# Performance work log

Hardware: AMD Instinct MI355X
Metric: run time of the kernel (lower is better)

## Reference

```python
import jax, jax.numpy as jnp
import numpy as np

HIDDEN = 64
N_NODES = 100000
N_EDGES = 1250000
EDGE_FEAT = 13


def setup_inputs() -> dict:
    key = jax.random.key(0)
    ks = jax.random.split(key, 16)
    d = HIDDEN
    inp = {
        'x': jax.random.normal(ks[0], (N_NODES, d), dtype=jnp.float32),
        'edge_index': jax.random.randint(ks[1], (2, N_EDGES), 0, N_NODES, dtype=jnp.int64),
        'edge_attr': jax.random.uniform(ks[2], (N_EDGES, EDGE_FEAT), dtype=jnp.float32),
        # learned params
        'aaaaa': jax.random.normal(ks[3], (EDGE_FEAT, 1), dtype=jnp.float32) * 0.5,
        'W1': jax.random.normal(ks[4], (d, d), dtype=jnp.float32) / np.sqrt(d),
        'b1': jnp.zeros((d,), dtype=jnp.float32),
        'W2': jax.random.normal(ks[5], (d, d), dtype=jnp.float32) / np.sqrt(d),
        'b2': jnp.zeros((d,), dtype=jnp.float32),
        'W3': jax.random.normal(ks[6], (d, d), dtype=jnp.float32) / np.sqrt(d),
        'b3': jnp.zeros((d,), dtype=jnp.float32),
        'wg1': jax.random.normal(ks[7], (d, 1), dtype=jnp.float32) / np.sqrt(d),
        'bg1': jnp.zeros((1,), dtype=jnp.float32),
        'wg2': jax.random.normal(ks[8], (d, 1), dtype=jnp.float32) / np.sqrt(d),
        'bg2': jnp.zeros((1,), dtype=jnp.float32),
        'wg3': jax.random.normal(ks[9], (d, 1), dtype=jnp.float32) / np.sqrt(d),
        'bg3': jnp.zeros((1,), dtype=jnp.float32),
    }
    return inp


def _gcn_norm(edge_index, edge_weight, num_nodes):
    # PyG gcn_norm: add self-loops (weight 1), symmetric deg^{-1/2} normalization
    loop = jnp.arange(num_nodes, dtype=edge_index.dtype)
    rows = jnp.concatenate([edge_index[0], loop])
    cols = jnp.concatenate([edge_index[1], loop])
    w = jnp.concatenate([edge_weight, jnp.ones((num_nodes,), edge_weight.dtype)])
    deg = jax.ops.segment_sum(w, cols, num_segments=num_nodes)
    dinv = jnp.where(deg > 0, jax.lax.rsqrt(jnp.where(deg > 0, deg, 1.0)), 0.0)
    norm = dinv[rows] * w * dinv[cols]
    return rows, cols, norm


def _gcn_layer(x, W, b, rows, cols, norm, num_nodes):
    h = x @ W  # transform first (out_dim == in_dim)
    msg = norm[:, None] * h[rows]          # gather + scale  [E+N, d]
    out = jnp.zeros_like(h).at[cols].add(msg)  # scatter-add aggregation
    return out + b


def _att_pool(x, wg, bg):
    # GlobalAttention with single graph (batch all zeros):
    # gate = sigmoid(Linear(x)); softmax over nodes; weighted sum
    gate = jax.nn.sigmoid(x @ wg + bg)      # [N, 1]
    a = jax.nn.softmax(gate, axis=0)        # softmax over node dim
    return jnp.sum(a * x, axis=0, keepdims=True)  # [1, d]


def reference(x, edge_index, edge_attr, aaaaa, W1, b1, W2, b2, W3, b3,
              wg1, bg1, wg2, bg2, wg3, bg3):
    num_nodes = x.shape[0]
    edge_weight = (edge_attr @ jax.nn.softmax(aaaaa, axis=0)).reshape(-1)  # [E]
    rows, cols, norm = _gcn_norm(edge_index, edge_weight, num_nodes)

    x1 = jax.nn.relu(_gcn_layer(x, W1, b1, rows, cols, norm, num_nodes))
    r1 = _att_pool(x1, wg1, bg1)
    x2 = jax.nn.relu(_gcn_layer(x1, W2, b2, rows, cols, norm, num_nodes))
    r2 = _att_pool(x2, wg2, bg2)
    x3 = jax.nn.relu(_gcn_layer(x2, W3, b3, rows, cols, norm, num_nodes))
    r3 = _att_pool(x3, wg3, bg3)
    return jnp.concatenate([r1, r2, r3], axis=1)  # [1, 3*hidden]
```

## Files before the change

### kernel.cpp

```cpp
#include <hip/hip_runtime.h>
#include <hip/hip_bf16.h>
#include <math.h>

#define HIDDEN    64
#define N_NODES   100000
#define N_EDGES   1250000
#define EDGE_FEAT 13

#define GATHER_BLOCKS 2048
#define GEMM_NB   ((N_NODES + 255) / 256)

#define NBKT    391
#define BCAP    4096
#define A_EPB   2048
#define NBLKA   ((N_EDGES + A_EPB - 1) / A_EPB)

typedef unsigned short bf16_t;
typedef unsigned char  u8;
typedef unsigned short u16;
typedef unsigned int   u32;
typedef unsigned long long u64;

#if defined(__has_builtin)
# if __has_builtin(__builtin_amdgcn_cvt_f32_fp8)
#  define USE_HW_FP8 1
# endif
#endif

static __device__ __forceinline__ float bf2f(bf16_t u) {
    union { unsigned int i; float f; } x; x.i = ((unsigned int)u) << 16; return x.f;
}
static __device__ __forceinline__ bf16_t f2bf(float f) {
    union { float f; unsigned int i; } u; u.f = f;
    unsigned int r = u.i + 0x7FFFu + ((u.i >> 16) & 1u);
    return (bf16_t)(r >> 16);
}

static __device__ __forceinline__ u8 f2fp8(float f) {
    union { float f; unsigned int u; } v; v.f = f;
    unsigned int s = (v.u >> 31) << 7;
    unsigned int mag = v.u & 0x7fffffffu;
    if (mag >= 0x43E80000u) return (u8)(s | 0x7Eu);
    if (mag < 0x3C800000u) {
        union { unsigned int u; float f; } t; t.u = mag;
        int qi = (int)rintf(t.f * 512.0f);
        return (u8)(s | (unsigned int)qi);
    }
    unsigned int r = mag + 0x7FFFFu + ((mag >> 20) & 1u);
    unsigned int e8 = (r >> 23) - 120u;
    unsigned int m3 = (r >> 20) & 7u;
    return (u8)(s | (e8 << 3) | m3);
}

static __device__ __forceinline__ float fp8dec(u32 b) {
#ifdef USE_HW_FP8
    return __builtin_amdgcn_cvt_f32_fp8(b, 0);
#else
    u32 m = b & 0x7Fu;
    u32 sgn = (b & 0x80u) << 24;
    union { u32 u; float f; } fn; fn.u = 0x3C000000u + (m << 20);
    float mg = (m < 8u) ? (float)m * (1.0f / 512.0f) : fn.f;
    union { float f; u32 u; } r; r.f = mg; r.u |= sgn;
    return r.f;
#endif
}

#define OFF_TOT    0
#define OFF_GBASE  2048
#define OFF_BLKH   4096
#define OFF_BLKE   960512
#define OFF_VST    1916928
#define OFF_START  1916928
#define OFF_DINV   2316928
#define OFF_ACC    2716928
#define OFF_POOLP  2717952
#define OFF_REC    4315392
#define OFF_H8     11916928
#define OFF_A      18316928
#define OFF_BREC   OFF_H8

__global__ __launch_bounds__(256) void wqk_kernel(
    const float* __restrict__ attr, const int* __restrict__ rows,
    const int* __restrict__ cols, const float* __restrict__ aaaaa,
    u64* __restrict__ vstash, int* __restrict__ blkHist, int E)
{
    __shared__ float s[16];
    __shared__ int hist[NBKT];
    int t = threadIdx.x, blk = blockIdx.x;
    if (t == 0) {
        float m = -1e30f;
        for (int i = 0; i < EDGE_FEAT; i++) m = fmaxf(m, aaaaa[i]);
        float ex[EDGE_FEAT]; float sum = 0.f;
        for (int i = 0; i < EDGE_FEAT; i++) { ex[i] = __expf(aaaaa[i] - m); sum += ex[i]; }
        float inv = 1.f / sum;
        for (int i = 0; i < EDGE_FEAT; i++) s[i] = ex[i] * inv;
    }
    for (int b = t; b < NBKT; b += 256) hist[b] = 0;
    __syncthreads();

    int e0 = blk * A_EPB;
    for (int c = 0; c < A_EPB / 256; c++) {
        int e = e0 + c * 256 + t;
        if (e < E) {
            const float* ap = attr + (size_t)e * EDGE_FEAT;
            float acc = 0.f;
#pragma unroll
            for (int f = 0; f < EDGE_FEAT; f++) acc = fmaf(ap[f], s[f], acc);
            u32 wq = min((u32)(fmaxf(acc, 0.f) * 32768.0f), 32767u);
            u32 cc = (u32)cols[e], rr = (u32)rows[e];
            int rk = atomicAdd(&hist[cc >> 8], 1);
            vstash[e] = ((u64)(u32)rk << 49) | ((u64)wq << 34) | ((u64)cc << 17) | (u64)rr;
        }
    }
    __syncthreads();
    for (int b = t; b < NBKT; b += 256) blkHist[blk * NBKT + b] = hist[b];
}

__global__ __launch_bounds__(256) void colscan_kernel(
    const int* __restrict__ blkHist, int* __restrict__ blkExcl,
    int* __restrict__ bucketTot)
{
    __shared__ int sv[768];
    int t = threadIdx.x, b = blockIdx.x;
    int v0 = (t < NBLKA) ? blkHist[(size_t)t * NBKT + b] : 0;
    int v1 = (t + 256 < NBLKA) ? blkHist[(size_t)(t + 256) * NBKT + b] : 0;
    int v2 = (t + 512 < NBLKA) ? blkHist[(size_t)(t + 512) * NBKT + b] : 0;
    sv[t] = v0; sv[t + 256] = v1; sv[t + 512] = v2;
    __syncthreads();
    for (int off = 1; off < 768; off <<= 1) {
        int a0 = (t >= off) ? sv[t - off] : 0;
        int a1 = (t + 256 >= off) ? sv[t + 256 - off] : 0;
        int a2 = sv[t + 512 - off];
        __syncthreads();
        sv[t] += a0; sv[t + 256] += a1; sv[t + 512] += a2;
        __syncthreads();
    }
    if (t < NBLKA) blkExcl[(size_t)t * NBKT + b] = sv[t] - v0;
    if (t + 256 < NBLKA) blkExcl[(size_t)(t + 256) * NBKT + b] = sv[t + 256] - v1;
    if (t + 512 < NBLKA) blkExcl[(size_t)(t + 512) * NBKT + b] = sv[t + 512] - v2;
    if (t == 0) bucketTot[b] = sv[NBLKA - 1];
}

__global__ void bscan(const int* __restrict__ bucketTot, int* __restrict__ gbase) {
    __shared__ int sc[512];
    int t = threadIdx.x;
    int v0 = (t < NBKT) ? bucketTot[t] : 0;
    int v1 = (t + 256 < NBKT) ? bucketTot[t + 256] : 0;
    sc[t] = v0; sc[t + 256] = v1;
    __syncthreads();
    for (int off = 1; off < 512; off <<= 1) {
        int a0 = (t >= off) ? sc[t - off] : 0;
        int a1 = sc[t + 256 - off];
        __syncthreads();
        sc[t] += a0; sc[t + 256] += a1;
        __syncthreads();
    }
    if (t < NBKT) gbase[t] = sc[t] - v0;
    if (t + 256 < NBKT) gbase[t + 256] = sc[t + 256] - v1;
}

__global__ __launch_bounds__(256) void scat_kernel(
    const u64* __restrict__ vstash, const int* __restrict__ blkHist,
    const int* __restrict__ blkExcl, u64* __restrict__ brec, int E)
{
    __shared__ u64 lbuf[A_EPB];
    __shared__ int hist[NBKT];
    __shared__ int exg[NBKT];
    __shared__ int cex[512];
    int t = threadIdx.x, blk = blockIdx.x;
    for (int b = t; b < NBKT; b += 256) {
        hist[b] = blkHist[(size_t)blk * NBKT + b];
        exg[b]  = blkExcl[(size_t)blk * NBKT + b];
    }
    __syncthreads();
    cex[t]       = (t < NBKT) ? hist[t] : 0;
    cex[t + 256] = (t + 256 < NBKT) ? hist[t + 256] : 0;
    __syncthreads();
    for (int off = 1; off < 512; off <<= 1) {
        int a0 = (t >= off) ? cex[t - off] : 0;
        int a1 = cex[t + 256 - off];
        __syncthreads();
        cex[t] += a0; cex[t + 256] += a1;
        __syncthreads();
    }

    int e0 = blk * A_EPB;
    int blkcnt = min(A_EPB, E - e0);
    for (int c = 0; c < A_EPB / 256; c++) {
        int e = e0 + c * 256 + t;
        if (e < E) {
            u64 v = vstash[e];
            int b = (int)((v >> 25) & 0x1FFu);
            int rk = (int)(v >> 49);
            lbuf[cex[b] - hist[b] + rk] = v;
        }
    }
    __syncthreads();
    for (int i = t; i < blkcnt; i += 256) {
        u64 w = lbuf[i];
        int b = (int)((w >> 25) & 0x1FFu);
        int ex = cex[b] - hist[b];
        int slot = exg[b] + (i - ex);
        if (slot < BCAP)
            brec[(size_t)b * BCAP + slot] = w;
    }
}

__global__ __launch_bounds__(256) void sortb_kernel(
    const u64* __restrict__ brec,
    const int* __restrict__ bucketTot, const int* __restrict__ gbase,
    u32* __restrict__ recp, int* __restrict__ startA,
    float* __restrict__ dinv, int N)
{
    __shared__ int hist[256];
    __shared__ int isum[256];
    __shared__ int incl[256];
    __shared__ u16 rnk[BCAP];
    __shared__ u64 buf[BCAP];
    int t = threadIdx.x;
    int b = blockIdx.x;
    int cnt = min(bucketTot[b], BCAP);
    int gb = gbase[b];
    int cbase = b << 8;
    int ncols = min(256, N - cbase);
    hist[t] = 0; isum[t] = 0;
    __syncthreads();

    for (int i = t; i < cnt; i += 256) {
        u64 v = brec[(size_t)b * BCAP + i];
        buf[i] = v;
        int c = (int)((v >> 17) & 255u);
        int wq = (int)((v >> 34) & 0x7FFFu);
        rnk[i] = (u16)atomicAdd(&hist[c], 1);
        atomicAdd(&isum[c], wq);
    }
    __syncthreads();

    incl[t] = hist[t];
    __syncthreads();
    for (int off = 1; off < 256; off <<= 1) {
        int a0 = (t >= off) ? incl[t - off] : 0;
        __syncthreads();
        incl[t] += a0;
        __syncthreads();
    }
    if (t < ncols) {
        startA[cbase + t] = gb + (incl[t] - hist[t]);
        dinv[cbase + t] = rsqrtf(1.0f + (float)isum[t] * (1.0f / 32768.0f));
    }
    __syncthreads();

    for (int i = t; i < cnt; i += 256) {
        u64 v = buf[i];
        int c = (int)((v >> 17) & 255u);
        int ex = incl[c] - hist[c];
        u32 row = (u32)(v & 0x1FFFFu);
        u32 wq = (u32)((v >> 34) & 0x7FFFu);
        recp[gb + ex + rnk[i]] = (row << 15) | wq;
    }
}

template <typename T> struct Feat;
template <> struct Feat<float> {
    static __device__ __forceinline__ float4 ld4(const float* A, size_t off) {
        return *(const float4*)(A + off);
    }
};
template <> struct Feat<bf16_t> {
    static __device__ __forceinline__ float4 ld4(const bf16_t* A, size_t off) {
        uint2 v = *(const uint2*)(A + off);
        float4 r;
        r.x = bf2f((bf16_t)(v.x & 0xffffu));
        r.y = bf2f((bf16_t)(v.x >> 16));
        r.z = bf2f((bf16_t)(v.y & 0xffffu));
        r.w = bf2f((bf16_t)(v.y >> 16));
        return r;
    }
};

template <typename TIn>
__global__ __launch_bounds__(256) void gemm64(const TIn* __restrict__ A,
                                              const float* __restrict__ W,
                                              const float* __restrict__ dinv,
                                              u8* __restrict__ H8, int N) {
    __shared__ float Ws[HIDDEN * HIDDEN];
    int tid = threadIdx.x;
    {
        const float4* Wv = (const float4*)W;
        float4* Sv = (float4*)Ws;
#pragma unroll
        for (int i = 0; i < 4; i++) Sv[tid + 256 * i] = Wv[tid + 256 * i];
    }
    __syncthreads();
    int rg = tid >> 2;
    int c0 = (tid & 3) * 16;
    int rbase = blockIdx.x * 256 + rg;
    int rld[4]; bool rok[4];
#pragma unroll
    for (int i = 0; i < 4; i++) {
        int r = rbase + 64 * i;
        rok[i] = (r < N);
        rld[i] = rok[i] ? r : 0;
    }
    float acc[4][16];
#pragma unroll
    for (int i = 0; i < 4; i++)
#pragma unroll
        for (int j = 0; j < 16; j++) acc[i][j] = 0.f;

    for (int k = 0; k < HIDDEN; k += 4) {
        float4 a4[4];
#pragma unroll
        for (int i = 0; i < 4; i++)
            a4[i] = Feat<TIn>::ld4(A, (size_t)rld[i] * HIDDEN + k);
#pragma unroll
        for (int kk = 0; kk < 4; kk++) {
            const float* wr = &Ws[(k + kk) * HIDDEN + c0];
            float4 W0 = *(const float4*)(wr);
            float4 W1 = *(const float4*)(wr + 4);
            float4 W2 = *(const float4*)(wr + 8);
            float4 W3 = *(const float4*)(wr + 12);
            float wv[16] = {W0.x, W0.y, W0.z, W0.w, W1.x, W1.y, W1.z, W1.w,
                            W2.x, W2.y, W2.z, W2.w, W3.x, W3.y, W3.z, W3.w};
#pragma unroll
            for (int i = 0; i < 4; i++) {
                float ak[4] = {a4[i].x, a4[i].y, a4[i].z, a4[i].w};
                float av = ak[kk];
#pragma unroll
                for (int j = 0; j < 16; j++) acc[i][j] = fmaf(av, wv[j], acc[i][j]);
            }
        }
    }
#pragma unroll
    for (int i = 0; i < 4; i++) {
        if (!rok[i]) continue;
        float dv = dinv[rld[i]];
        unsigned int wd[4];
#pragma unroll
        for (int q = 0; q < 4; q++) {
            unsigned int b0 = f2fp8(dv * acc[i][4*q]);
            unsigned int b1 = f2fp8(dv * acc[i][4*q+1]);
            unsigned int b2 = f2fp8(dv * acc[i][4*q+2]);
            unsigned int b3 = f2fp8(dv * acc[i][4*q+3]);
            wd[q] = b0 | (b1 << 8) | (b2 << 16) | (b3 << 24);
        }
        *(uint4*)(H8 + (size_t)rld[i] * HIDDEN + c0) = make_uint4(wd[0], wd[1], wd[2], wd[3]);
    }
}

__global__ __launch_bounds__(256) void gather_pool_kernel(
    const u8* __restrict__ h8,
    const int* __restrict__ start,
    const u32* __restrict__ recp,
    const float* __restrict__ dinv, const float* __restrict__ bias,
    const float* __restrict__ wg, const float* __restrict__ bg,
    bf16_t* __restrict__ out, float* __restrict__ poolpart, int N)
{
    __shared__ float sred[4][65];
    int lane = threadIdx.x & 63;
    int wid  = threadIdx.x >> 6;
    int wave = blockIdx.x * 4 + wid;
    const int nwaves = GATHER_BLOCKS * 4;
    float wgv = wg[lane];
    float bg0 = bg[0];
    float bv  = bias[lane];
    float accv = 0.f, accs = 0.f;

    for (int n = wave; n < N; n += nwaves) {
        int s = start[n];
        int e2 = (n + 1 < N) ? start[n + 1] : N_EDGES;
        float di = dinv[n];
        float a0 = fp8dec(h8[(u32)(n * HIDDEN + lane)]);
        float a1 = 0.f, a2 = 0.f, a3 = 0.f;
        for (int base = s; base < e2; base += 64) {
            int cnt64 = min(e2 - base, 64);
            u32 rv = recp[base + min(lane, cnt64 - 1)];
            for (int j = 0; j < cnt64; j += 8) {
                float hv[8], wt[8];
#pragma unroll
                for (int jj = 0; jj < 8; jj++) {
                    int q = j + jj;
                    int qq = (q < cnt64) ? q : (cnt64 - 1);
                    u32 p = (u32)__shfl((int)rv, qq, 64);
                    wt[jj] = (q < cnt64) ? (float)(p & 0x7FFFu) * (1.0f / 32768.0f) : 0.f;
                    hv[jj] = fp8dec(h8[(p >> 15) * (u32)HIDDEN + (u32)lane]);
                }
                a0 = fmaf(wt[0], hv[0], a0);
                a1 = fmaf(wt[1], hv[1], a1);
                a2 = fmaf(wt[2], hv[2], a2);
                a3 = fmaf(wt[3], hv[3], a3);
                a0 = fmaf(wt[4], hv[4], a0);
                a1 = fmaf(wt[5], hv[5], a1);
                a2 = fmaf(wt[6], hv[6], a2);
                a3 = fmaf(wt[7], hv[7], a3);
            }
        }
        float v = fmaxf(fmaf(di, (a0 + a1) + (a2 + a3), bv), 0.f);
        out[(size_t)n * HIDDEN + lane] = f2bf(v);
        float p = v * wgv;
#pragma unroll
        for (int m = 32; m > 0; m >>= 1) p += __shfl_xor(p, m, 64);
        float g = 1.f / (1.f + __expf(-(p + bg0)));
        float eg = __expf(g);
        accv = fmaf(eg, v, accv);
        accs += eg;
    }

    sred[wid][lane] = accv;
    if (lane == 0) sred[wid][64] = accs;
    __syncthreads();
    if (wid == 0) {
        float s0 = sred[0][lane] + sred[1][lane] + sred[2][lane] + sred[3][lane];
        poolpart[(size_t)lane * GATHER_BLOCKS + blockIdx.x] = s0;
        if (lane == 0) {
            float ss = sred[0][64] + sred[1][64] + sred[2][64] + sred[3][64];
            poolpart[(size_t)64 * GATHER_BLOCKS + blockIdx.x] = ss;
        }
    }
}

__global__ void pool_reduce(const float* __restrict__ poolpart, float* __restrict__ acc) {
    int entry = (int)((blockIdx.x * blockDim.x + threadIdx.x) >> 6);
    int lane = threadIdx.x & 63;
    if (entry >= 3 * 65) return;
    const float* p = poolpart + (size_t)entry * GATHER_BLOCKS;
    float s = 0.f;
    for (int i = lane; i < GATHER_BLOCKS; i += 64) s += p[i];
#pragma unroll
    for (int m = 32; m > 0; m >>= 1) s += __shfl_xor(s, m, 64);
    if (lane == 0) acc[entry] = s;
}

__global__ void finalize_kernel(const float* __restrict__ acc, float* __restrict__ out) {
    int i = threadIdx.x;
    if (i >= 3 * HIDDEN) return;
    int layer = i >> 6, c = i & 63;
    const float* a = acc + layer * 65;
    out[i] = a[c] / a[64];
}

extern "C" void kernel_launch(void* const* d_in, const int* in_sizes, int n_in,
                              void* d_out, int out_size, void* d_ws, size_t ws_size,
                              hipStream_t stream) {
    const float* x          = (const float*)d_in[0];
    const int*   edge_index = (const int*)  d_in[1];
    const float* edge_attr  = (const float*)d_in[2];
    const float* aaaaa      = (const float*)d_in[3];
    const float* W1 = (const float*)d_in[4];  const float* b1 = (const float*)d_in[5];
    const float* W2 = (const float*)d_in[6];  const float* b2 = (const float*)d_in[7];
    const float* W3 = (const float*)d_in[8];  const float* b3 = (const float*)d_in[9];
    const float* wg1 = (const float*)d_in[10]; const float* bg1 = (const float*)d_in[11];
    const float* wg2 = (const float*)d_in[12]; const float* bg2 = (const float*)d_in[13];
    const float* wg3 = (const float*)d_in[14]; const float* bg3 = (const float*)d_in[15];
    float* out = (float*)d_out;

    char* ws = (char*)d_ws;
    int*    bucketTot = (int*)   (ws + OFF_TOT);
    int*    gbase     = (int*)   (ws + OFF_GBASE);
    int*    blkHist   = (int*)   (ws + OFF_BLKH);
    int*    blkExcl   = (int*)   (ws + OFF_BLKE);
    u64*    vstash    = (u64*)   (ws + OFF_VST);
    int*    startA    = (int*)   (ws + OFF_START);
    float*  dinv      = (float*) (ws + OFF_DINV);
    float*  acc       = (float*) (ws + OFF_ACC);
    float*  poolpart  = (float*) (ws + OFF_POOLP);
    u32*    recp      = (u32*)   (ws + OFF_REC);
    u8*     h8        = (u8*)    (ws + OFF_H8);
    bf16_t* bufA      = (bf16_t*)(ws + OFF_A);
    u64*    brec      = (u64*)   (ws + OFF_BREC);

    const int* rows = edge_index;
    const int* cols = edge_index + N_EDGES;
    const int N = N_NODES, E = N_EDGES;

    wqk_kernel<<<NBLKA, 256, 0, stream>>>(edge_attr, rows, cols, aaaaa, vstash, blkHist, E);
    colscan_kernel<<<NBKT, 256, 0, stream>>>(blkHist, blkExcl, bucketTot);
    bscan<<<1, 256, 0, stream>>>(bucketTot, gbase);
    scat_kernel<<<NBLKA, 256, 0, stream>>>(vstash, blkHist, blkExcl, brec, E);
    sortb_kernel<<<NBKT, 256, 0, stream>>>(brec, bucketTot, gbase, recp, startA, dinv, N);

    const float* Wm[3]  = {W1, W2, W3};
    const float* bs[3]  = {b1, b2, b3};
    const float* wgs[3] = {wg1, wg2, wg3};
    const float* bgs[3] = {bg1, bg2, bg3};

    for (int l = 0; l < 3; l++) {
        if (l == 0)
            gemm64<float><<<GEMM_NB, 256, 0, stream>>>(x, Wm[l], dinv, h8, N);
        else
            gemm64<bf16_t><<<GEMM_NB, 256, 0, stream>>>(bufA, Wm[l], dinv, h8, N);
        gather_pool_kernel<<<GATHER_BLOCKS, 256, 0, stream>>>(
            h8, startA, recp, dinv, bs[l], wgs[l], bgs[l],
            bufA, poolpart + (size_t)l * 65 * GATHER_BLOCKS, N);
    }

    pool_reduce<<<(3 * 65 * 64 + 255) / 256, 256, 0, stream>>>(poolpart, acc);
    finalize_kernel<<<1, 192, 0, stream>>>(acc, out);
}
```

Measured before the change: 418.3 us.

## Gather fp8 rows as 4-byte words across 4 edge slots; stage edge attrs in LDS

```diff
diff --git a/kernel.cpp b/kernel.cpp
--- a/kernel.cpp
+++ b/kernel.cpp
@@ -20,10 +20,14 @@
 typedef unsigned short u16;
 typedef unsigned int   u32;
 typedef unsigned long long u64;
+typedef float f32x2 __attribute__((ext_vector_type(2)));
 
 #if defined(__has_builtin)
 # if __has_builtin(__builtin_amdgcn_cvt_f32_fp8)
 #  define USE_HW_FP8 1
+# endif
+# if __has_builtin(__builtin_amdgcn_cvt_pk_f32_fp8)
+#  define USE_HW_FP8PK 1
 # endif
 #endif
 
@@ -62,6 +66,19 @@
     float mg = (m < 8u) ? (float)m * (1.0f / 512.0f) : fn.f;
     union { float f; u32 u; } r; r.f = mg; r.u |= sgn;
     return r.f;
+#endif
+}
+
+static __device__ __forceinline__ void fp8x4dec(u32 w, float* f) {
+#ifdef USE_HW_FP8PK
+    f32x2 lo = __builtin_amdgcn_cvt_pk_f32_fp8(w, false);
+    f32x2 hi = __builtin_amdgcn_cvt_pk_f32_fp8(w, true);
+    f[0] = lo.x; f[1] = lo.y; f[2] = hi.x; f[3] = hi.y;
+#else
+    f[0] = fp8dec(w & 0xFFu);
+    f[1] = fp8dec((w >> 8) & 0xFFu);
+    f[2] = fp8dec((w >> 16) & 0xFFu);
+    f[3] = fp8dec((w >> 24) & 0xFFu);
 #endif
 }
 
@@ -86,6 +103,7 @@
 {
     __shared__ float s[16];
     __shared__ int hist[NBKT];
+    __shared__ float astage[EDGE_FEAT * 256];
     int t = threadIdx.x, blk = blockIdx.x;
     if (t == 0) {
         float m = -1e30f;
@@ -99,20 +117,30 @@
     __syncthreads();
 
     int e0 = blk * A_EPB;
+#pragma unroll 1
     for (int c = 0; c < A_EPB / 256; c++) {
-        int e = e0 + c * 256 + t;
+        int ebase = e0 + c * 256;
+        int lim = (min(256, E - ebase)) * EDGE_FEAT;
+        size_t gb = (size_t)ebase * EDGE_FEAT;
+#pragma unroll
+        for (int j = 0; j < EDGE_FEAT; j++) {
+            int idx = t + j * 256;
+            if (idx < lim) astage[idx] = attr[gb + idx];
+        }
+        __syncthreads();
+        int e = ebase + t;
         if (e < E) {
-            const float* ap = attr + (size_t)e * EDGE_FEAT;
+            const float* rowp = &astage[t * EDGE_FEAT];
             float acc = 0.f;
 #pragma unroll
-            for (int f = 0; f < EDGE_FEAT; f++) acc = fmaf(ap[f], s[f], acc);
+            for (int f = 0; f < EDGE_FEAT; f++) acc = fmaf(rowp[f], s[f], acc);
             u32 wq = min((u32)(fmaxf(acc, 0.f) * 32768.0f), 32767u);
             u32 cc = (u32)cols[e], rr = (u32)rows[e];
             int rk = atomicAdd(&hist[cc >> 8], 1);
             vstash[e] = ((u64)(u32)rk << 49) | ((u64)wq << 34) | ((u64)cc << 17) | (u64)rr;
         }
-    }
-    __syncthreads();
+        __syncthreads();
+    }
     for (int b = t; b < NBKT; b += 256) blkHist[blk * NBKT + b] = hist[b];
 }
 
@@ -357,56 +385,84 @@
     bf16_t* __restrict__ out, float* __restrict__ poolpart, int N)
 {
     __shared__ float sred[4][65];
-    int lane = threadIdx.x & 63;
-    int wid  = threadIdx.x >> 6;
+    int lane  = threadIdx.x & 63;
+    int wid   = threadIdx.x >> 6;
+    int eslot = lane >> 4;
+    int ch4   = (lane & 15) * 4;
     int wave = blockIdx.x * 4 + wid;
     const int nwaves = GATHER_BLOCKS * 4;
-    float wgv = wg[lane];
+    float4 wgv = *(const float4*)(wg + ch4);
+    float4 bv4 = *(const float4*)(bias + ch4);
     float bg0 = bg[0];
-    float bv  = bias[lane];
-    float accv = 0.f, accs = 0.f;
+    float accv[4] = {0.f, 0.f, 0.f, 0.f};
+    float accs = 0.f;
 
     for (int n = wave; n < N; n += nwaves) {
         int s = start[n];
         int e2 = (n + 1 < N) ? start[n + 1] : N_EDGES;
         float di = dinv[n];
-        float a0 = fp8dec(h8[(u32)(n * HIDDEN + lane)]);
-        float a1 = 0.f, a2 = 0.f, a3 = 0.f;
+        float a[4] = {0.f, 0.f, 0.f, 0.f};
         for (int base = s; base < e2; base += 64) {
             int cnt64 = min(e2 - base, 64);
             u32 rv = recp[base + min(lane, cnt64 - 1)];
             for (int j = 0; j < cnt64; j += 8) {
-                float hv[8], wt[8];
-#pragma unroll
-                for (int jj = 0; jj < 8; jj++) {
-                    int q = j + jj;
-                    int qq = (q < cnt64) ? q : (cnt64 - 1);
-                    u32 p = (u32)__shfl((int)rv, qq, 64);
-                    wt[jj] = (q < cnt64) ? (float)(p & 0x7FFFu) * (1.0f / 32768.0f) : 0.f;
-                    hv[jj] = fp8dec(h8[(p >> 15) * (u32)HIDDEN + (u32)lane]);
+                int q0 = j + eslot, q1 = j + 4 + eslot;
+                u32 p0 = (u32)__shfl((int)rv, q0 & 63, 64);
+                u32 p1 = (u32)__shfl((int)rv, q1 & 63, 64);
+                float w0 = (q0 < cnt64) ? (float)(p0 & 0x7FFFu) : 0.f;
+                float w1 = (q1 < cnt64) ? (float)(p1 & 0x7FFFu) : 0.f;
+                u32 off0 = ((p0 & 0xFFFF8000u) >> 9) + (u32)ch4;
+                u32 off1 = ((p1 & 0xFFFF8000u) >> 9) + (u32)ch4;
+                u32 d0 = *(const u32*)(h8 + off0);
+                u32 d1 = *(const u32*)(h8 + off1);
+                float h0[4], h1[4];
+                fp8x4dec(d0, h0);
+                fp8x4dec(d1, h1);
+#pragma unroll
+                for (int i = 0; i < 4; i++) {
+                    a[i] = fmaf(w0, h0[i], a[i]);
+                    a[i] = fmaf(w1, h1[i], a[i]);
                 }
-                a0 = fmaf(wt[0], hv[0], a0);
-                a1 = fmaf(wt[1], hv[1], a1);
-                a2 = fmaf(wt[2], hv[2], a2);
-                a3 = fmaf(wt[3], hv[3], a3);
-                a0 = fmaf(wt[4], hv[4], a0);
-                a1 = fmaf(wt[5], hv[5], a1);
-                a2 = fmaf(wt[6], hv[6], a2);
-                a3 = fmaf(wt[7], hv[7], a3);
             }
         }
-        float v = fmaxf(fmaf(di, (a0 + a1) + (a2 + a3), bv), 0.f);
-        out[(size_t)n * HIDDEN + lane] = f2bf(v);
-        float p = v * wgv;
-#pragma unroll
-        for (int m = 32; m > 0; m >>= 1) p += __shfl_xor(p, m, 64);
+#pragma unroll
+        for (int i = 0; i < 4; i++) {
+            a[i] += __shfl_xor(a[i], 16, 64);
+            a[i] += __shfl_xor(a[i], 32, 64);
+        }
+        u32 sw = *(const u32*)(h8 + (u32)n * (u32)HIDDEN + (u32)ch4);
+        float sf[4];
+        fp8x4dec(sw, sf);
+        float dis = di * (1.0f / 32768.0f);
+        float v[4];
+#pragma unroll
+        for (int i = 0; i < 4; i++) {
+            float t0 = fmaf(dis, a[i], ((const float*)&bv4)[i]);
+            v[i] = fmaxf(fmaf(di, sf[i], t0), 0.f);
+        }
+        if (eslot == 0) {
+            u32 lo = (u32)f2bf(v[0]) | ((u32)f2bf(v[1]) << 16);
+            u32 hi = (u32)f2bf(v[2]) | ((u32)f2bf(v[3]) << 16);
+            *(uint2*)(out + (size_t)n * HIDDEN + ch4) = make_uint2(lo, hi);
+        }
+        float p = v[0] * wgv.x + v[1] * wgv.y + v[2] * wgv.z + v[3] * wgv.w;
+        p += __shfl_xor(p, 1, 64);
+        p += __shfl_xor(p, 2, 64);
+        p += __shfl_xor(p, 4, 64);
+        p += __shfl_xor(p, 8, 64);
         float g = 1.f / (1.f + __expf(-(p + bg0)));
         float eg = __expf(g);
-        accv = fmaf(eg, v, accv);
+#pragma unroll
+        for (int i = 0; i < 4; i++) accv[i] = fmaf(eg, v[i], accv[i]);
         accs += eg;
     }
 
-    sred[wid][lane] = accv;
+    if (eslot == 0) {
+        sred[wid][ch4 + 0] = accv[0];
+        sred[wid][ch4 + 1] = accv[1];
+        sred[wid][ch4 + 2] = accv[2];
+        sred[wid][ch4 + 3] = accv[3];
+    }
     if (lane == 0) sred[wid][64] = accs;
     __syncthreads();
     if (wid == 0) {
```

New measurement: 416.9 us. About the same (-0.3%).
